# Performance work log

Hardware: AMD Instinct MI355X
Metric: run time of the kernel (lower is better)

Reference implementation:

```python
import jax, jax.numpy as jnp
import numpy as np

B, T, N, C = 2, 8, 50000, 64
HID, R, L, E = 128, 16, 12, 1600000


def setup_inputs() -> dict:
    key = jax.random.key(0)
    ks = jax.random.split(key, 12)
    X = jax.random.normal(ks[0], (B, T, N, C), dtype=jnp.float32)
    edge_index = jax.random.randint(ks[1], (2, E), 0, N, dtype=jnp.int64)
    s = 1.0 / np.sqrt(C)
    s2 = 1.0 / np.sqrt(HID)
    W1s = jax.random.uniform(ks[2], (C, HID), jnp.float32, -s, s)
    b1s = jax.random.uniform(ks[3], (HID,), jnp.float32, -s, s)
    W2s = jax.random.uniform(ks[4], (HID, R), jnp.float32, -s2, s2)
    b2s = jax.random.uniform(ks[5], (R,), jnp.float32, -0.01, 0.01)
    W1d = jax.random.uniform(ks[6], (C, HID), jnp.float32, -s, s)
    b1d = jax.random.uniform(ks[7], (HID,), jnp.float32, -s, s)
    W2d = jax.random.uniform(ks[8], (HID, R), jnp.float32, -s2, s2)
    b2d = jax.random.uniform(ks[9], (R,), jnp.float32, -0.01, 0.01)
    gamma = jax.random.uniform(ks[10], (L, R), jnp.float32, 0.01, 0.05)
    return {"X": X, "edge_index": edge_index,
            "W1s": W1s, "b1s": b1s, "W2s": W2s, "b2s": b2s,
            "W1d": W1d, "b1d": b1d, "W2d": W2d, "b2d": b2d,
            "gamma": gamma}


def reference(X, edge_index, W1s, b1s, W2s, b2s, W1d, b1d, W2d, b2d, gamma):
    # pooling='last': H is (B, N, C)
    H = X[:, -1]
    # node MLP embeddings (B, N, r)
    a = jax.nn.relu(H @ W1s + b1s) @ W2s + b2s
    b = jax.nn.relu(H @ W1d + b1d) @ W2d + b2d
    I, J = edge_index[0], edge_index[1]
    a_i = a[:, I]  # (B, E, r) gather over src nodes
    b_j = b[:, J]  # (B, E, r) gather over dst nodes
    # diag mix: logits[b,l,e] = sum_r a_i[b,e,r] * gamma[l,r] * b_j[b,e,r]
    logits = jnp.einsum('ber,lr,ber->ble', a_i, gamma, b_j)
    return logits
```

## Files before the change

kernel.cpp:

```cpp
#include <hip/hip_runtime.h>


typedef unsigned short u16;
typedef unsigned int   u32;
typedef __attribute__((ext_vector_type(8))) short short8;
typedef __attribute__((ext_vector_type(4))) float f32x4;

#define N_NODES 50000
#define T_STEPS 8
#define C_DIM   64
#define HID     128
#define R_DIM   16
#define L_DIM   12
#define E_EDGES 1600000
#define TILES   6250
#define HSTRIDE 136
#define W1S     72
#define W2S     136
#define TAB_U16 ((size_t)N_NODES * 32)

__device__ __forceinline__ float bf2f(u16 u) {
  unsigned v = ((unsigned)u) << 16;
  return __builtin_bit_cast(float, v);
}
__device__ __forceinline__ u16 f2bf(float f) {
  unsigned x = __builtin_bit_cast(unsigned, f);
  x += 0x7fffu + ((x >> 16) & 1u);
  return (u16)(x >> 16);
}
__device__ __forceinline__ u16 ld_bf(const void* p, int idx, bool f32) {
  return f32 ? f2bf(((const float*)p)[idx]) : ((const u16*)p)[idx];
}
__device__ __forceinline__ float ld_f(const void* p, int idx, bool f32) {
  return f32 ? ((const float*)p)[idx] : bf2f(((const u16*)p)[idx]);
}

__global__ __launch_bounds__(256) void detect_kernel(
    const u16* __restrict__ w1u, const u32* __restrict__ eraw, int* flags)
{
  __shared__ int cnt, zcnt;
  const int t = threadIdx.x;
  if (t == 0) { cnt = 0; zcnt = 0; }
  __syncthreads();
  int c = 0;
#pragma unroll
  for (int i = 0; i < 8; ++i) {
    u16 u = w1u[t * 8 + i];
    int e = (u >> 7) & 0xFF;
    if (e >= 100 && e <= 127) c++;
  }
  atomicAdd(&cnt, c);
  if (t < 64 && eraw[2 * t + 1] == 0) atomicAdd(&zcnt, 1);
  __syncthreads();
  if (t == 0) {
    flags[0] = (cnt < 1638) ? 1 : 0;
    flags[1] = (zcnt == 64) ? 1 : 0;
  }
}

__global__ __launch_bounds__(256, 2) void mlp_kernel(
    const void* __restrict__ X,
    const void* __restrict__ W1s, const void* __restrict__ b1s,
    const void* __restrict__ W2s, const void* __restrict__ b2s,
    const void* __restrict__ W1d, const void* __restrict__ b1d,
    const void* __restrict__ W2d, const void* __restrict__ b2d,
    u16* __restrict__ Atb, u16* __restrict__ Btb,
    const int* __restrict__ flags)
{
  __shared__ u16 w1t[2 * HID * W1S];
  __shared__ u16 w2t[2 * R_DIM * W2S];
  __shared__ u16 hidb[4 * 16 * HSTRIDE];
  __shared__ float b1l[2 * HID];
  __shared__ float b2l[2 * R_DIM];

  const bool isf32 = flags[0] != 0;
  const int tid  = threadIdx.x;
  const int wave = tid >> 6;
  const int lane = tid & 63;
  const int nl   = lane & 15;
  const int quad = lane >> 4;

  const void* W1p[2] = {W1s, W1d};
  const void* W2p[2] = {W2s, W2d};
  const void* b1p[2] = {b1s, b1d};
  const void* b2p[2] = {b2s, b2d};

#pragma unroll
  for (int m = 0; m < 2; ++m) {
    for (int f = tid; f < C_DIM * HID; f += 256) {
      int k = f >> 7, n = f & 127;
      w1t[m * HID * W1S + n * W1S + k] = ld_bf(W1p[m], f, isf32);
    }
    for (int f = tid; f < HID * R_DIM; f += 256) {
      int k = f >> 4, r = f & 15;
      w2t[m * R_DIM * W2S + r * W2S + k] = ld_bf(W2p[m], f, isf32);
    }
    if (tid < HID)   b1l[m * HID + tid]   = ld_f(b1p[m], tid, isf32);
    if (tid < R_DIM) b2l[m * R_DIM + tid] = ld_f(b2p[m], tid, isf32);
  }
  __syncthreads();

  float b1v[2][8], b2v[2];
#pragma unroll
  for (int m = 0; m < 2; ++m) {
#pragma unroll
    for (int ct = 0; ct < 8; ++ct) b1v[m][ct] = b1l[m * HID + ct * 16 + nl];
    b2v[m] = b2l[m * R_DIM + nl];
  }

  u16* hw = hidb + wave * 16 * HSTRIDE;

  for (int tile = blockIdx.x * 4 + wave; tile < TILES; tile += gridDim.x * 4) {
    const int g0 = tile * 16;
    const int g = g0 + nl;
    const int bb = (g >= N_NODES) ? 1 : 0;
    const int n = g - bb * N_NODES;
    const size_t rowoff = ((size_t)(bb * T_STEPS + T_STEPS - 1) * N_NODES + n) * C_DIM;

    short8 af0, af1;
    if (isf32) {
      const float* xf = (const float*)X + rowoff;
#pragma unroll
      for (int j = 0; j < 8; ++j) {
        af0[j] = (short)f2bf(xf[quad * 8 + j]);
        af1[j] = (short)f2bf(xf[32 + quad * 8 + j]);
      }
    } else {
      const u16* xb = (const u16*)X + rowoff;
      af0 = *(const short8*)(xb + quad * 8);
      af1 = *(const short8*)(xb + 32 + quad * 8);
    }

#pragma unroll
    for (int m = 0; m < 2; ++m) {
      const u16* w1m = w1t + m * HID * W1S;
#pragma unroll
      for (int ct = 0; ct < 8; ++ct) {
        f32x4 acc = {b1v[m][ct], b1v[m][ct], b1v[m][ct], b1v[m][ct]};
        short8 bf0 = *(const short8*)(w1m + (ct * 16 + nl) * W1S + quad * 8);
        short8 bf1 = *(const short8*)(w1m + (ct * 16 + nl) * W1S + 32 + quad * 8);
        acc = __builtin_amdgcn_mfma_f32_16x16x32_bf16(af0, bf0, acc, 0, 0, 0);
        acc = __builtin_amdgcn_mfma_f32_16x16x32_bf16(af1, bf1, acc, 0, 0, 0);
#pragma unroll
        for (int i = 0; i < 4; ++i) {
          float h = acc[i] > 0.f ? acc[i] : 0.f;
          hw[(quad * 4 + i) * HSTRIDE + ct * 16 + nl] = f2bf(h);
        }
      }
      const u16* w2m = w2t + m * R_DIM * W2S;
      f32x4 acc2 = {b2v[m], b2v[m], b2v[m], b2v[m]};
#pragma unroll
      for (int kt = 0; kt < 4; ++kt) {
        short8 a2  = *(const short8*)(hw + nl * HSTRIDE + kt * 32 + quad * 8);
        short8 b2f = *(const short8*)(w2m + nl * W2S + kt * 32 + quad * 8);
        acc2 = __builtin_amdgcn_mfma_f32_16x16x32_bf16(a2, b2f, acc2, 0, 0, 0);
      }
      u16* outp = (m == 0) ? Atb : Btb;
#pragma unroll
      for (int i = 0; i < 4; ++i) {
        int gg = g0 + quad * 4 + i;
        int bo = (gg >= N_NODES) ? 1 : 0;
        int nn = gg - bo * N_NODES;
        outp[(size_t)nn * 32 + bo * 16 + nl] = f2bf(acc2[i]);
      }
    }
  }
}

__global__ __launch_bounds__(256, 4) void edge_kernel(
    const void* __restrict__ eidx,
    const u16* __restrict__ Atb, const u16* __restrict__ Btb,
    const void* __restrict__ gamma, void* __restrict__ out,
    const int* __restrict__ flags)
{
  __shared__ float gf[L_DIM * R_DIM];
  const bool isf32 = flags[0] != 0;
  const bool isi64 = flags[1] != 0;
  const int tid = threadIdx.x;
  if (tid < L_DIM * R_DIM) gf[tid] = ld_f(gamma, tid, isf32);
  __syncthreads();

  const int e = blockIdx.x * 256 + tid;
  int inode, jnode;
  if (isi64) {
    const long long* p = (const long long*)eidx;
    inode = (int)p[e]; jnode = (int)p[E_EDGES + e];
  } else {
    const int* p = (const int*)eidx;
    inode = p[e]; jnode = p[E_EDGES + e];
  }

  const short8* ar = (const short8*)(Atb + (size_t)inode * 32);
  const short8* br = (const short8*)(Btb + (size_t)jnode * 32);
  short8 a0 = ar[0], a1 = ar[1], a2 = ar[2], a3 = ar[3];
  short8 b0 = br[0], b1 = br[1], b2 = br[2], b3 = br[3];

  float p0[16], p1[16];
#pragma unroll
  for (int j = 0; j < 8; ++j) {
    p0[j]     = bf2f((u16)a0[j]) * bf2f((u16)b0[j]);
    p0[8 + j] = bf2f((u16)a1[j]) * bf2f((u16)b1[j]);
    p1[j]     = bf2f((u16)a2[j]) * bf2f((u16)b2[j]);
    p1[8 + j] = bf2f((u16)a3[j]) * bf2f((u16)b3[j]);
  }

#pragma unroll
  for (int l = 0; l < L_DIM; ++l) {
    float s0 = 0.f, s1 = 0.f;
#pragma unroll
    for (int r = 0; r < R_DIM; ++r) {
      float g = gf[l * R_DIM + r];
      s0 += g * p0[r];
      s1 += g * p1[r];
    }
    size_t i0 = (size_t)l * E_EDGES + e;
    size_t i1 = (size_t)(L_DIM + l) * E_EDGES + e;
    if (isf32) {
      ((float*)out)[i0] = s0; ((float*)out)[i1] = s1;
    } else {
      ((u16*)out)[i0] = f2bf(s0); ((u16*)out)[i1] = f2bf(s1);
    }
  }
}

extern "C" void kernel_launch(void* const* d_in, const int* in_sizes, int n_in,
                              void* d_out, int out_size, void* d_ws, size_t ws_size,
                              hipStream_t stream) {
  const void* X     = d_in[0];
  const void* eidx  = d_in[1];
  const void* W1s   = d_in[2];
  const void* b1s   = d_in[3];
  const void* W2s   = d_in[4];
  const void* b2s   = d_in[5];
  const void* W1d   = d_in[6];
  const void* b1d   = d_in[7];
  const void* W2d   = d_in[8];
  const void* b2d   = d_in[9];
  const void* gamma = d_in[10];

  u16* Atb   = (u16*)d_ws;
  u16* Btb   = Atb + TAB_U16;
  int* flags = (int*)(Btb + TAB_U16);

  hipLaunchKernelGGL(detect_kernel, dim3(1), dim3(256), 0, stream,
                     (const u16*)W1s, (const u32*)eidx, flags);
  hipLaunchKernelGGL(mlp_kernel, dim3(512), dim3(256), 0, stream,
                     X, W1s, b1s, W2s, b2s, W1d, b1d, W2d, b2d, Atb, Btb, flags);
  hipLaunchKernelGGL(edge_kernel, dim3(E_EDGES / 256), dim3(256), 0, stream,
                     eidx, Atb, Btb, gamma, d_out, flags);
}
```

Measured before the change: 389.0 us.

## Fold dtype detection into MLP kernel, vectorize loads, two edges per thread

Removes the separate single-block detect kernel and has every MLP block recompute the dtype flags itself, with block 0 writing them for the edge kernel. X rows are read with vectorized nontemporal loads. The edge kernel now handles two edges per thread, with vectorized index loads and paired nontemporal output stores, and launches half as many blocks. This aims to cut one launch and raise memory-access width, at the cost of higher register pressure and redundant detection work in each block.

```diff
diff --git a/kernel.cpp b/kernel.cpp
--- a/kernel.cpp
+++ b/kernel.cpp
@@ -5,6 +5,9 @@
 typedef unsigned int   u32;
 typedef __attribute__((ext_vector_type(8))) short short8;
 typedef __attribute__((ext_vector_type(4))) float f32x4;
+typedef __attribute__((ext_vector_type(2))) float f32x2;
+typedef __attribute__((ext_vector_type(2))) long long ll2;
+typedef __attribute__((ext_vector_type(2))) int i32x2;
 
 #define N_NODES 50000
 #define T_STEPS 8
@@ -35,50 +38,48 @@
   return f32 ? ((const float*)p)[idx] : bf2f(((const u16*)p)[idx]);
 }
 
-__global__ __launch_bounds__(256) void detect_kernel(
-    const u16* __restrict__ w1u, const u32* __restrict__ eraw, int* flags)
-{
-  __shared__ int cnt, zcnt;
-  const int t = threadIdx.x;
-  if (t == 0) { cnt = 0; zcnt = 0; }
-  __syncthreads();
-  int c = 0;
-#pragma unroll
-  for (int i = 0; i < 8; ++i) {
-    u16 u = w1u[t * 8 + i];
-    int e = (u >> 7) & 0xFF;
-    if (e >= 100 && e <= 127) c++;
-  }
-  atomicAdd(&cnt, c);
-  if (t < 64 && eraw[2 * t + 1] == 0) atomicAdd(&zcnt, 1);
-  __syncthreads();
-  if (t == 0) {
-    flags[0] = (cnt < 1638) ? 1 : 0;
-    flags[1] = (zcnt == 64) ? 1 : 0;
-  }
-}
-
 __global__ __launch_bounds__(256, 2) void mlp_kernel(
-    const void* __restrict__ X,
+    const void* __restrict__ X, const void* __restrict__ eidx,
     const void* __restrict__ W1s, const void* __restrict__ b1s,
     const void* __restrict__ W2s, const void* __restrict__ b2s,
     const void* __restrict__ W1d, const void* __restrict__ b1d,
     const void* __restrict__ W2d, const void* __restrict__ b2d,
     u16* __restrict__ Atb, u16* __restrict__ Btb,
-    const int* __restrict__ flags)
+    int* __restrict__ flags)
 {
   __shared__ u16 w1t[2 * HID * W1S];
   __shared__ u16 w2t[2 * R_DIM * W2S];
   __shared__ u16 hidb[4 * 16 * HSTRIDE];
   __shared__ float b1l[2 * HID];
   __shared__ float b2l[2 * R_DIM];
-
-  const bool isf32 = flags[0] != 0;
+  __shared__ int s_cnt, s_zcnt;
+
   const int tid  = threadIdx.x;
   const int wave = tid >> 6;
   const int lane = tid & 63;
   const int nl   = lane & 15;
   const int quad = lane >> 4;
+
+  if (tid == 0) { s_cnt = 0; s_zcnt = 0; }
+  __syncthreads();
+  {
+    int c = 0;
+    const u16* w1u = (const u16*)W1s;
+#pragma unroll
+    for (int i = 0; i < 8; ++i) {
+      u16 u = w1u[tid * 8 + i];
+      int ex = (u >> 7) & 0xFF;
+      if (ex >= 100 && ex <= 127) c++;
+    }
+    atomicAdd(&s_cnt, c);
+    if (tid < 64 && ((const u32*)eidx)[2 * tid + 1] == 0) atomicAdd(&s_zcnt, 1);
+  }
+  __syncthreads();
+  const bool isf32 = s_cnt < 1638;
+  if (blockIdx.x == 0 && tid == 0) {
+    flags[0] = isf32 ? 1 : 0;
+    flags[1] = (s_zcnt == 64) ? 1 : 0;
+  }
 
   const void* W1p[2] = {W1s, W1d};
   const void* W2p[2] = {W2s, W2d};
@@ -120,15 +121,21 @@
     short8 af0, af1;
     if (isf32) {
       const float* xf = (const float*)X + rowoff;
-#pragma unroll
-      for (int j = 0; j < 8; ++j) {
-        af0[j] = (short)f2bf(xf[quad * 8 + j]);
-        af1[j] = (short)f2bf(xf[32 + quad * 8 + j]);
+      f32x4 x0 = __builtin_nontemporal_load((const f32x4*)(xf + quad * 8));
+      f32x4 x1 = __builtin_nontemporal_load((const f32x4*)(xf + quad * 8 + 4));
+      f32x4 x2 = __builtin_nontemporal_load((const f32x4*)(xf + 32 + quad * 8));
+      f32x4 x3 = __builtin_nontemporal_load((const f32x4*)(xf + 32 + quad * 8 + 4));
+#pragma unroll
+      for (int j = 0; j < 4; ++j) {
+        af0[j]     = (short)f2bf(x0[j]);
+        af0[4 + j] = (short)f2bf(x1[j]);
+        af1[j]     = (short)f2bf(x2[j]);
+        af1[4 + j] = (short)f2bf(x3[j]);
       }
     } else {
       const u16* xb = (const u16*)X + rowoff;
-      af0 = *(const short8*)(xb + quad * 8);
-      af1 = *(const short8*)(xb + 32 + quad * 8);
+      af0 = __builtin_nontemporal_load((const short8*)(xb + quad * 8));
+      af1 = __builtin_nontemporal_load((const short8*)(xb + 32 + quad * 8));
     }
 
 #pragma unroll
@@ -180,45 +187,65 @@
   if (tid < L_DIM * R_DIM) gf[tid] = ld_f(gamma, tid, isf32);
   __syncthreads();
 
-  const int e = blockIdx.x * 256 + tid;
-  int inode, jnode;
+  const int e0 = (blockIdx.x * 256 + tid) * 2;
+  int inode0, inode1, jnode0, jnode1;
   if (isi64) {
-    const long long* p = (const long long*)eidx;
-    inode = (int)p[e]; jnode = (int)p[E_EDGES + e];
+    ll2 vi = __builtin_nontemporal_load((const ll2*)((const long long*)eidx + e0));
+    ll2 vj = __builtin_nontemporal_load((const ll2*)((const long long*)eidx + E_EDGES + e0));
+    inode0 = (int)vi[0]; inode1 = (int)vi[1];
+    jnode0 = (int)vj[0]; jnode1 = (int)vj[1];
   } else {
-    const int* p = (const int*)eidx;
-    inode = p[e]; jnode = p[E_EDGES + e];
-  }
-
-  const short8* ar = (const short8*)(Atb + (size_t)inode * 32);
-  const short8* br = (const short8*)(Btb + (size_t)jnode * 32);
-  short8 a0 = ar[0], a1 = ar[1], a2 = ar[2], a3 = ar[3];
-  short8 b0 = br[0], b1 = br[1], b2 = br[2], b3 = br[3];
-
-  float p0[16], p1[16];
-#pragma unroll
-  for (int j = 0; j < 8; ++j) {
-    p0[j]     = bf2f((u16)a0[j]) * bf2f((u16)b0[j]);
-    p0[8 + j] = bf2f((u16)a1[j]) * bf2f((u16)b1[j]);
-    p1[j]     = bf2f((u16)a2[j]) * bf2f((u16)b2[j]);
-    p1[8 + j] = bf2f((u16)a3[j]) * bf2f((u16)b3[j]);
-  }
-
-#pragma unroll
+    i32x2 vi = __builtin_nontemporal_load((const i32x2*)((const int*)eidx + e0));
+    i32x2 vj = __builtin_nontemporal_load((const i32x2*)((const int*)eidx + E_EDGES + e0));
+    inode0 = vi[0]; inode1 = vi[1];
+    jnode0 = vj[0]; jnode1 = vj[1];
+  }
+
+  float p0[2][16], p1[2][16];
+#pragma unroll
+  for (int s = 0; s < 2; ++s) {
+    const int in = s ? inode1 : inode0;
+    const int jn = s ? jnode1 : jnode0;
+    const short8* ar = (const short8*)(Atb + (size_t)in * 32);
+    const short8* br = (const short8*)(Btb + (size_t)jn * 32);
+    short8 a0 = ar[0], a1 = ar[1], a2 = ar[2], a3 = ar[3];
+    short8 b0 = br[0], b1 = br[1], b2 = br[2], b3 = br[3];
+#pragma unroll
+    for (int j = 0; j < 8; ++j) {
+      p0[s][j]     = bf2f((u16)a0[j]) * bf2f((u16)b0[j]);
+      p0[s][8 + j] = bf2f((u16)a1[j]) * bf2f((u16)b1[j]);
+      p1[s][j]     = bf2f((u16)a2[j]) * bf2f((u16)b2[j]);
+      p1[s][8 + j] = bf2f((u16)a3[j]) * bf2f((u16)b3[j]);
+    }
+  }
+
+  float* outf = (float*)out;
+  u16*   outh = (u16*)out;
+#pragma unroll 2
   for (int l = 0; l < L_DIM; ++l) {
-    float s0 = 0.f, s1 = 0.f;
-#pragma unroll
-    for (int r = 0; r < R_DIM; ++r) {
-      float g = gf[l * R_DIM + r];
-      s0 += g * p0[r];
-      s1 += g * p1[r];
-    }
-    size_t i0 = (size_t)l * E_EDGES + e;
-    size_t i1 = (size_t)(L_DIM + l) * E_EDGES + e;
+    const f32x4* gr = (const f32x4*)(gf + l * R_DIM);
+    f32x4 g0 = gr[0], g1 = gr[1], g2 = gr[2], g3 = gr[3];
+    float s00 = 0.f, s01 = 0.f, s10 = 0.f, s11 = 0.f;
+#pragma unroll
+    for (int r = 0; r < 16; ++r) {
+      float g = (r < 4) ? g0[r] : (r < 8) ? g1[r - 4] : (r < 12) ? g2[r - 8] : g3[r - 12];
+      s00 = fmaf(g, p0[0][r], s00);
+      s01 = fmaf(g, p0[1][r], s01);
+      s10 = fmaf(g, p1[0][r], s10);
+      s11 = fmaf(g, p1[1][r], s11);
+    }
+    size_t o0 = (size_t)l * E_EDGES + e0;
+    size_t o1 = (size_t)(L_DIM + l) * E_EDGES + e0;
     if (isf32) {
-      ((float*)out)[i0] = s0; ((float*)out)[i1] = s1;
+      f32x2 v0 = {s00, s01};
+      f32x2 v1 = {s10, s11};
+      __builtin_nontemporal_store(v0, (f32x2*)(outf + o0));
+      __builtin_nontemporal_store(v1, (f32x2*)(outf + o1));
     } else {
-      ((u16*)out)[i0] = f2bf(s0); ((u16*)out)[i1] = f2bf(s1);
+      u32 w0 = (u32)f2bf(s00) | ((u32)f2bf(s01) << 16);
+      u32 w1 = (u32)f2bf(s10) | ((u32)f2bf(s11) << 16);
+      __builtin_nontemporal_store(w0, (u32*)(outh + o0));
+      __builtin_nontemporal_store(w1, (u32*)(outh + o1));
     }
   }
 }
@@ -242,10 +269,8 @@
   u16* Btb   = Atb + TAB_U16;
   int* flags = (int*)(Btb + TAB_U16);
 
-  hipLaunchKernelGGL(detect_kernel, dim3(1), dim3(256), 0, stream,
-                     (const u16*)W1s, (const u32*)eidx, flags);
   hipLaunchKernelGGL(mlp_kernel, dim3(512), dim3(256), 0, stream,
-                     X, W1s, b1s, W2s, b2s, W1d, b1d, W2d, b2d, Atb, Btb, flags);
-  hipLaunchKernelGGL(edge_kernel, dim3(E_EDGES / 256), dim3(256), 0, stream,
+                     X, eidx, W1s, b1s, W2s, b2s, W1d, b1d, W2d, b2d, Atb, Btb, flags);
+  hipLaunchKernelGGL(edge_kernel, dim3(E_EDGES / 512), dim3(256), 0, stream,
                      eidx, Atb, Btb, gamma, d_out, flags);
 }
```

After: 393.3 us. Within noise of the previous version (+1.1%).
